# Kernel optimization log

Hardware: AMD Instinct MI355X
Metric: run time of the kernel (lower is better)

Reference implementation:

```python
import jax, jax.numpy as jnp
import numpy as np

NUM_TEAMS = 100000
INPUT_SIZE = 128
HIDDEN = 128
NUM_MATCHES = 1000000
OUT = 3


def setup_inputs() -> dict:
    key = jax.random.key(0)
    ks = jax.random.split(key, 10)
    s_ih = 1.0 / np.sqrt(HIDDEN)
    inputs = jax.random.normal(ks[0], (NUM_TEAMS, INPUT_SIZE), dtype=jnp.float32)
    hx = jax.random.normal(ks[1], (NUM_TEAMS, HIDDEN), dtype=jnp.float32)
    cx = jax.random.normal(ks[2], (NUM_TEAMS, HIDDEN), dtype=jnp.float32)
    matches = jax.random.randint(ks[3], (NUM_MATCHES, 2), 0, NUM_TEAMS, dtype=jnp.int64)
    W_ih = jax.random.uniform(ks[4], (4 * HIDDEN, INPUT_SIZE), jnp.float32, -s_ih, s_ih)
    W_hh = jax.random.uniform(ks[5], (4 * HIDDEN, HIDDEN), jnp.float32, -s_ih, s_ih)
    b_ih = jax.random.uniform(ks[6], (4 * HIDDEN,), jnp.float32, -s_ih, s_ih)
    b_hh = jax.random.uniform(ks[7], (4 * HIDDEN,), jnp.float32, -s_ih, s_ih)
    s_o = 1.0 / np.sqrt(2 * HIDDEN)
    W_out = jax.random.uniform(ks[8], (OUT, 2 * HIDDEN), jnp.float32, -s_o, s_o)
    b_out = jax.random.uniform(ks[9], (OUT,), jnp.float32, -s_o, s_o)
    return {"inputs": inputs, "hx": hx, "cx": cx, "matches": matches,
            "W_ih": W_ih, "W_hh": W_hh, "b_ih": b_ih, "b_hh": b_hh,
            "W_out": W_out, "b_out": b_out}


def reference(inputs, hx, cx, matches, W_ih, W_hh, b_ih, b_hh, W_out, b_out):
    # Batched LSTMCell step across all teams (replaces per-team Python loop).
    gates = inputs @ W_ih.T + b_ih + hx @ W_hh.T + b_hh  # [T, 4H]
    i_g, f_g, g_g, o_g = jnp.split(gates, 4, axis=1)
    c_new = jax.nn.sigmoid(f_g) * cx + jax.nn.sigmoid(i_g) * jnp.tanh(g_g)
    h_new = jax.nn.sigmoid(o_g) * jnp.tanh(c_new)  # [T, H]
    # Fused gather + concat + linear + softmax for all matches.
    home = h_new[matches[:, 0]]  # [M, H]
    away = h_new[matches[:, 1]]  # [M, H]
    feat = jnp.concatenate([home, away], axis=1)  # [M, 2H]
    logits = feat @ W_out.T + b_out  # [M, 3]
    pmf = jax.nn.softmax(logits, axis=-1)
    return pmf
```

## Files before the change

kernel.cpp:

```cpp
#include <hip/hip_runtime.h>
#include <hip/hip_bf16.h>

typedef __bf16 bf16x8 __attribute__((ext_vector_type(8)));
typedef float f32x4 __attribute__((ext_vector_type(4)));

#define NUM_TEAMS 100000
#define NUM_MATCHES 1000000
#define LOG2E 1.4426950408889634f
#define NWG 6250
#define XQ 781
#define XR 2

__device__ __forceinline__ unsigned short f2bf(float x) {
    __hip_bfloat16 h = __float2bfloat16(x);
    return reinterpret_cast<unsigned short&>(h);
}
__device__ __forceinline__ unsigned int cvtpk(float a, float b) {
    unsigned int r;
    asm("v_cvt_pk_bf16_f32 %0, %1, %2" : "=v"(r) : "v"(a), "v"(b));
    return r;
}
__device__ __forceinline__ float exp2_(float x) {
    float r; asm("v_exp_f32 %0, %1" : "=v"(r) : "v"(x)); return r;
}
__device__ __forceinline__ float rcp_(float x) {
    float r; asm("v_rcp_f32 %0, %1" : "=v"(r) : "v"(x)); return r;
}
__device__ __forceinline__ void load_lds16(const float* g, float* l) {
    __builtin_amdgcn_global_load_lds(
        (const __attribute__((address_space(1))) void*)g,
        (__attribute__((address_space(3))) void*)l, 16, 0, 0);
}

__global__ __launch_bounds__(256) void prep_kernel(
    const float* __restrict__ W_ih, const float* __restrict__ W_hh,
    const float* __restrict__ b_ih, const float* __restrict__ b_hh,
    unsigned short* __restrict__ Wpk, float* __restrict__ biasc)
{
    int gid = blockIdx.x * 256 + threadIdx.x;
    int e = gid & 7;
    int chunk = gid >> 3;
    int l15 = chunk & 15;
    int l4 = (chunk >> 4) & 3;
    int rest = chunk >> 6;
    int ks = rest & 7;
    int gate = (rest >> 3) & 3;
    int G = rest >> 5;
    int row = gate * 128 + G * 16 + l15;
    int k = ks * 32 + l4 * 8 + e;
    float v = (k < 128) ? W_ih[row * 128 + k] : W_hh[row * 128 + (k - 128)];
    Wpk[gid] = f2bf(v);
    if (gid < 512) {
        float b = b_ih[gid] + b_hh[gid];
        float scale = ((gid >> 7) == 2) ? (2.0f * LOG2E) : (-LOG2E);
        biasc[gid] = b * scale;
    }
}

__global__ __launch_bounds__(256, 5) void lstm_kernel(
    const float* __restrict__ inputs, const float* __restrict__ hx,
    const float* __restrict__ cx, const unsigned short* __restrict__ Wpk,
    const float* __restrict__ biasc, const float* __restrict__ W_out,
    float* __restrict__ projP)
{
    __shared__ __align__(16) unsigned short Abf[32 * 256];
    __shared__ __align__(16) float cxl[8 * 260];
    __shared__ float Wlds[768];
    const int tid = threadIdx.x;

    const int orig = blockIdx.x;
    const int xcd = orig & 7, idx = orig >> 3;
    const int wgid = (xcd < XR ? xcd * (XQ + 1) : XR * (XQ + 1) + (xcd - XR) * XQ) + idx;
    const int tile = wgid >> 1, ch = wgid & 1;
    const int brow = tile * 32;

    const int lane = tid & 63;
    const int w = tid >> 6;
    const int l15 = lane & 15, l4 = lane >> 4;
    const int hl = w * 16 + l15;
    const int hcol = ch * 64 + hl;

    {
        #pragma unroll
        for (int p = 0; p < 2; ++p) {
            int team = brow + p * 16 + w * 4 + l4;
            load_lds16(cx + (size_t)team * 128 + ch * 64 + l15 * 4,
                       cxl + (p * 4 + w) * 260 + lane * 4);
        }
    }

    {
        const int r0 = tid >> 4, seg = tid & 15;
        const float* srcb = (seg < 8) ? inputs + seg * 16 : hx + (seg - 8) * 16;
        char* lbw = reinterpret_cast<char*>(Abf);
        const int swz = (r0 & 7) << 4;
        #pragma unroll
        for (int p = 0; p < 2; ++p) {
            int r = p * 16 + r0;
            const float* src = srcb + (size_t)(brow + r) * 128;
            float4 v0 = *reinterpret_cast<const float4*>(src);
            float4 v1 = *reinterpret_cast<const float4*>(src + 4);
            float4 v2 = *reinterpret_cast<const float4*>(src + 8);
            float4 v3 = *reinterpret_cast<const float4*>(src + 12);
            int base = r * 512 + seg * 32;
            uint4 q0, q1;
            q0.x = cvtpk(v0.x, v0.y); q0.y = cvtpk(v0.z, v0.w);
            q0.z = cvtpk(v1.x, v1.y); q0.w = cvtpk(v1.z, v1.w);
            q1.x = cvtpk(v2.x, v2.y); q1.y = cvtpk(v2.z, v2.w);
            q1.z = cvtpk(v3.x, v3.y); q1.w = cvtpk(v3.z, v3.w);
            *reinterpret_cast<uint4*>(lbw + (base ^ swz)) = q0;
            *reinterpret_cast<uint4*>(lbw + ((base + 16) ^ swz)) = q1;
        }
        Wlds[tid] = W_out[tid];
        Wlds[256 + tid] = W_out[256 + tid];
        Wlds[512 + tid] = W_out[512 + tid];
    }

    const unsigned short* bpg = Wpk + (size_t)(ch * 4 + w) * 16384 + lane * 8;
    const float bic = biasc[hcol];
    const float bfc = biasc[128 + hcol];
    const float bgc = biasc[256 + hcol];
    const float boc = biasc[384 + hcol];
    const int swzA = (l15 & 7) << 4;
    const int kf = l4 * 16;
    const char* pArow = reinterpret_cast<const char*>(Abf) + l15 * 512;

    f32x4 acc[2][4] = {};

    __syncthreads();

    #pragma unroll
    for (int ks = 0; ks < 8; ++ks) {
        bf16x8 b0 = *(const bf16x8*)(bpg + ks * 512);
        bf16x8 b1 = *(const bf16x8*)(bpg + 4096 + ks * 512);
        bf16x8 b2 = *(const bf16x8*)(bpg + 8192 + ks * 512);
        bf16x8 b3 = *(const bf16x8*)(bpg + 12288 + ks * 512);
        const int ko = (ks * 64 + kf) ^ swzA;
        #pragma unroll
        for (int m = 0; m < 2; ++m) {
            bf16x8 af = *(const bf16x8*)(pArow + m * 8192 + ko);
            acc[m][0] = __builtin_amdgcn_mfma_f32_16x16x32_bf16(af, b0, acc[m][0], 0, 0, 0);
            acc[m][1] = __builtin_amdgcn_mfma_f32_16x16x32_bf16(af, b1, acc[m][1], 0, 0, 0);
            acc[m][2] = __builtin_amdgcn_mfma_f32_16x16x32_bf16(af, b2, acc[m][2], 0, 0, 0);
            acc[m][3] = __builtin_amdgcn_mfma_f32_16x16x32_bf16(af, b3, acc[m][3], 0, 0, 0);
        }
    }

    __syncthreads();

    {
        char* lb = reinterpret_cast<char*>(Abf);
        #pragma unroll
        for (int m = 0; m < 2; ++m) {
            #pragma unroll
            for (int j = 0; j < 4; ++j) {
                float cxv = cxl[(m * 4 + l4) * 260 + j * 64 + hl];
                float si = rcp_(1.0f + exp2_(fmaf(acc[m][0][j], -LOG2E, bic)));
                float sf = rcp_(1.0f + exp2_(fmaf(acc[m][1][j], -LOG2E, bfc)));
                float tg = fmaf(-2.0f, rcp_(1.0f + exp2_(fmaf(acc[m][2][j], 2.0f * LOG2E, bgc))), 1.0f);
                float so = rcp_(1.0f + exp2_(fmaf(acc[m][3][j], -LOG2E, boc)));
                float cn = fmaf(sf, cxv, si * tg);
                float tc = fmaf(-2.0f, rcp_(1.0f + exp2_(cn * (2.0f * LOG2E))), 1.0f);
                float hn = so * tc;
                int t = m * 16 + l4 * 4 + j;
                *reinterpret_cast<float*>(lb + ((t * 256 + hl * 4) ^ ((t & 7) << 4))) = hn;
            }
        }
    }
    __syncthreads();

    {
        int tl = tid >> 3, sub = tid & 7;
        const char* lb = reinterpret_cast<const char*>(Abf);
        int hbase = tl * 256 + sub * 32;
        int hswz = (tl & 7) << 4;
        float a0 = 0.f, a1 = 0.f, a2 = 0.f, a3 = 0.f, a4 = 0.f, a5 = 0.f;
        #pragma unroll
        for (int c = 0; c < 2; ++c) {
            f32x4 h4 = *reinterpret_cast<const f32x4*>(lb + ((hbase + c * 16) ^ hswz));
            #pragma unroll
            for (int i = 0; i < 4; ++i) {
                float h = h4[i];
                int col = ch * 64 + sub * 8 + c * 4 + i;
                a0 += h * Wlds[col];       a1 += h * Wlds[256 + col]; a2 += h * Wlds[512 + col];
                a3 += h * Wlds[128 + col]; a4 += h * Wlds[384 + col]; a5 += h * Wlds[640 + col];
            }
        }
        a0 += __shfl_xor(a0, 1); a1 += __shfl_xor(a1, 1); a2 += __shfl_xor(a2, 1);
        a3 += __shfl_xor(a3, 1); a4 += __shfl_xor(a4, 1); a5 += __shfl_xor(a5, 1);
        a0 += __shfl_xor(a0, 2); a1 += __shfl_xor(a1, 2); a2 += __shfl_xor(a2, 2);
        a3 += __shfl_xor(a3, 2); a4 += __shfl_xor(a4, 2); a5 += __shfl_xor(a5, 2);
        a0 += __shfl_xor(a0, 4); a1 += __shfl_xor(a1, 4); a2 += __shfl_xor(a2, 4);
        a3 += __shfl_xor(a3, 4); a4 += __shfl_xor(a4, 4); a5 += __shfl_xor(a5, 4);
        int team = brow + tl;
        if (sub == 0) {
            float4* o = reinterpret_cast<float4*>(projP + (size_t)team * 16 + ch * 8);
            o[0] = make_float4(a0, a1, a2, a2);
            o[1] = make_float4(a3, a4, a5, a5);
        }
    }
}

__global__ __launch_bounds__(256) void match_kernel(
    const int* __restrict__ matches, const float* __restrict__ projP,
    const float* __restrict__ b_out, float* __restrict__ out)
{
    int m = blockIdx.x * 256 + threadIdx.x;
    if (m >= NUM_MATCHES) return;
    int2 mi = reinterpret_cast<const int2*>(matches)[m];
    const float4* pp = reinterpret_cast<const float4*>(projP);
    float4 h0 = pp[(size_t)mi.x * 4 + 0];
    float4 h1 = pp[(size_t)mi.x * 4 + 2];
    float4 a0 = pp[(size_t)mi.y * 4 + 1];
    float4 a1 = pp[(size_t)mi.y * 4 + 3];
    float l0 = h0.x + h1.x + a0.x + a1.x + b_out[0];
    float l1 = h0.y + h1.y + a0.y + a1.y + b_out[1];
    float l2 = h0.z + h1.z + a0.z + a1.z + b_out[2];
    float mx = fmaxf(l0, fmaxf(l1, l2));
    float e0 = __expf(l0 - mx), e1 = __expf(l1 - mx), e2 = __expf(l2 - mx);
    float inv = 1.0f / (e0 + e1 + e2);
    out[3 * m + 0] = e0 * inv;
    out[3 * m + 1] = e1 * inv;
    out[3 * m + 2] = e2 * inv;
}

extern "C" void kernel_launch(void* const* d_in, const int* in_sizes, int n_in,
                              void* d_out, int out_size, void* d_ws, size_t ws_size,
                              hipStream_t stream) {
    const float* inputs = (const float*)d_in[0];
    const float* hx     = (const float*)d_in[1];
    const float* cx     = (const float*)d_in[2];
    const int*   matches= (const int*)d_in[3];
    const float* W_ih   = (const float*)d_in[4];
    const float* W_hh   = (const float*)d_in[5];
    const float* b_ih   = (const float*)d_in[6];
    const float* b_hh   = (const float*)d_in[7];
    const float* W_out  = (const float*)d_in[8];
    const float* b_out  = (const float*)d_in[9];
    float* out = (float*)d_out;

    char* ws = (char*)d_ws;
    unsigned short* Wpk  = (unsigned short*)ws;
    float* biasc         = (float*)(ws + 262144);
    float* projP         = (float*)(ws + (1 << 20));

    prep_kernel <<<512, 256, 0, stream>>>(W_ih, W_hh, b_ih, b_hh, Wpk, biasc);
    lstm_kernel <<<NWG, 256, 0, stream>>>(inputs, hx, cx, Wpk, biasc, W_out, projP);
    match_kernel<<<(NUM_MATCHES + 255) / 256, 256, 0, stream>>>(matches, projP, b_out, out);
}
```

Baseline: 82.12 us.

## Compute both hidden halves per workgroup and halve projection gather traffic

Each workgroup now handles all 128 hidden columns of its 32-team tile in two passes instead of splitting the columns across two workgroups. The two half-projections are summed in registers, so projP shrinks to 8 floats per team and the match kernel gathers two float4 per match instead of four. cx is now read straight into registers instead of through an async LDS load, and each tile's inputs and hx rows are converted to bf16 only once. In exchange the grid is halved, which lowers parallelism, and each workgroup runs longer with more serialised MFMA and activation work.

Measured after the change: 156.0 us. 1.9x slower.

```diff
diff --git a/kernel.cpp b/kernel.cpp
--- a/kernel.cpp
+++ b/kernel.cpp
@@ -7,9 +7,9 @@
 #define NUM_TEAMS 100000
 #define NUM_MATCHES 1000000
 #define LOG2E 1.4426950408889634f
-#define NWG 6250
-#define XQ 781
-#define XR 2
+#define NWG 3125
+#define XQ 390
+#define XR 5
 
 __device__ __forceinline__ unsigned short f2bf(float x) {
     __hip_bfloat16 h = __float2bfloat16(x);
@@ -25,11 +25,6 @@
 }
 __device__ __forceinline__ float rcp_(float x) {
     float r; asm("v_rcp_f32 %0, %1" : "=v"(r) : "v"(x)); return r;
-}
-__device__ __forceinline__ void load_lds16(const float* g, float* l) {
-    __builtin_amdgcn_global_load_lds(
-        (const __attribute__((address_space(1))) void*)g,
-        (__attribute__((address_space(3))) void*)l, 16, 0, 0);
 }
 
 __global__ __launch_bounds__(256) void prep_kernel(
@@ -64,140 +59,156 @@
     float* __restrict__ projP)
 {
     __shared__ __align__(16) unsigned short Abf[32 * 256];
-    __shared__ __align__(16) float cxl[8 * 260];
+    __shared__ __align__(16) float Hf[32 * 64];
     __shared__ float Wlds[768];
     const int tid = threadIdx.x;
 
     const int orig = blockIdx.x;
     const int xcd = orig & 7, idx = orig >> 3;
-    const int wgid = (xcd < XR ? xcd * (XQ + 1) : XR * (XQ + 1) + (xcd - XR) * XQ) + idx;
-    const int tile = wgid >> 1, ch = wgid & 1;
+    const int tile = (xcd < XR ? xcd * (XQ + 1) : XR * (XQ + 1) + (xcd - XR) * XQ) + idx;
     const int brow = tile * 32;
 
     const int lane = tid & 63;
     const int w = tid >> 6;
     const int l15 = lane & 15, l4 = lane >> 4;
     const int hl = w * 16 + l15;
-    const int hcol = ch * 64 + hl;
 
     {
-        #pragma unroll
-        for (int p = 0; p < 2; ++p) {
-            int team = brow + p * 16 + w * 4 + l4;
-            load_lds16(cx + (size_t)team * 128 + ch * 64 + l15 * 4,
-                       cxl + (p * 4 + w) * 260 + lane * 4);
-        }
-    }
-
-    {
-        const int r0 = tid >> 4, seg = tid & 15;
-        const float* srcb = (seg < 8) ? inputs + seg * 16 : hx + (seg - 8) * 16;
+        const int r = tid >> 3, seg = tid & 7;
+        const float* src = ((seg < 4) ? inputs + seg * 32 : hx + (seg - 4) * 32)
+                           + (size_t)(brow + r) * 128;
+        float4 v0 = *reinterpret_cast<const float4*>(src);
+        float4 v1 = *reinterpret_cast<const float4*>(src + 4);
+        float4 v2 = *reinterpret_cast<const float4*>(src + 8);
+        float4 v3 = *reinterpret_cast<const float4*>(src + 12);
+        float4 v4 = *reinterpret_cast<const float4*>(src + 16);
+        float4 v5 = *reinterpret_cast<const float4*>(src + 20);
+        float4 v6 = *reinterpret_cast<const float4*>(src + 24);
+        float4 v7 = *reinterpret_cast<const float4*>(src + 28);
         char* lbw = reinterpret_cast<char*>(Abf);
-        const int swz = (r0 & 7) << 4;
-        #pragma unroll
-        for (int p = 0; p < 2; ++p) {
-            int r = p * 16 + r0;
-            const float* src = srcb + (size_t)(brow + r) * 128;
-            float4 v0 = *reinterpret_cast<const float4*>(src);
-            float4 v1 = *reinterpret_cast<const float4*>(src + 4);
-            float4 v2 = *reinterpret_cast<const float4*>(src + 8);
-            float4 v3 = *reinterpret_cast<const float4*>(src + 12);
-            int base = r * 512 + seg * 32;
-            uint4 q0, q1;
-            q0.x = cvtpk(v0.x, v0.y); q0.y = cvtpk(v0.z, v0.w);
-            q0.z = cvtpk(v1.x, v1.y); q0.w = cvtpk(v1.z, v1.w);
-            q1.x = cvtpk(v2.x, v2.y); q1.y = cvtpk(v2.z, v2.w);
-            q1.z = cvtpk(v3.x, v3.y); q1.w = cvtpk(v3.z, v3.w);
-            *reinterpret_cast<uint4*>(lbw + (base ^ swz)) = q0;
-            *reinterpret_cast<uint4*>(lbw + ((base + 16) ^ swz)) = q1;
-        }
+        const int base = r * 512 + seg * 64;
+        const int swz = (r & 7) << 4;
+        uint4 q0, q1;
+        q0.x = cvtpk(v0.x, v0.y); q0.y = cvtpk(v0.z, v0.w);
+        q0.z = cvtpk(v1.x, v1.y); q0.w = cvtpk(v1.z, v1.w);
+        q1.x = cvtpk(v2.x, v2.y); q1.y = cvtpk(v2.z, v2.w);
+        q1.z = cvtpk(v3.x, v3.y); q1.w = cvtpk(v3.z, v3.w);
+        *reinterpret_cast<uint4*>(lbw + (base ^ swz)) = q0;
+        *reinterpret_cast<uint4*>(lbw + ((base + 16) ^ swz)) = q1;
+        q0.x = cvtpk(v4.x, v4.y); q0.y = cvtpk(v4.z, v4.w);
+        q0.z = cvtpk(v5.x, v5.y); q0.w = cvtpk(v5.z, v5.w);
+        q1.x = cvtpk(v6.x, v6.y); q1.y = cvtpk(v6.z, v6.w);
+        q1.z = cvtpk(v7.x, v7.y); q1.w = cvtpk(v7.z, v7.w);
+        *reinterpret_cast<uint4*>(lbw + ((base + 32) ^ swz)) = q0;
+        *reinterpret_cast<uint4*>(lbw + ((base + 48) ^ swz)) = q1;
         Wlds[tid] = W_out[tid];
         Wlds[256 + tid] = W_out[256 + tid];
         Wlds[512 + tid] = W_out[512 + tid];
     }
 
-    const unsigned short* bpg = Wpk + (size_t)(ch * 4 + w) * 16384 + lane * 8;
-    const float bic = biasc[hcol];
-    const float bfc = biasc[128 + hcol];
-    const float bgc = biasc[256 + hcol];
-    const float boc = biasc[384 + hcol];
+    float cxa[8];
+    #pragma unroll
+    for (int m = 0; m < 2; ++m)
+        #pragma unroll
+        for (int j = 0; j < 4; ++j)
+            cxa[m * 4 + j] = cx[(size_t)(brow + m * 16 + l4 * 4 + j) * 128 + hl];
+
     const int swzA = (l15 & 7) << 4;
     const int kf = l4 * 16;
     const char* pArow = reinterpret_cast<const char*>(Abf) + l15 * 512;
 
-    f32x4 acc[2][4] = {};
+    float p0, p1, p2, p3, p4, p5;
 
     __syncthreads();
 
     #pragma unroll
-    for (int ks = 0; ks < 8; ++ks) {
-        bf16x8 b0 = *(const bf16x8*)(bpg + ks * 512);
-        bf16x8 b1 = *(const bf16x8*)(bpg + 4096 + ks * 512);
-        bf16x8 b2 = *(const bf16x8*)(bpg + 8192 + ks * 512);
-        bf16x8 b3 = *(const bf16x8*)(bpg + 12288 + ks * 512);
-        const int ko = (ks * 64 + kf) ^ swzA;
+    for (int ch = 0; ch < 2; ++ch) {
+        const int hcol = ch * 64 + hl;
+        const unsigned short* bpg = Wpk + (size_t)(ch * 4 + w) * 16384 + lane * 8;
+        const float bic = biasc[hcol];
+        const float bfc = biasc[128 + hcol];
+        const float bgc = biasc[256 + hcol];
+        const float boc = biasc[384 + hcol];
+
+        f32x4 acc[2][4] = {};
         #pragma unroll
-        for (int m = 0; m < 2; ++m) {
-            bf16x8 af = *(const bf16x8*)(pArow + m * 8192 + ko);
-            acc[m][0] = __builtin_amdgcn_mfma_f32_16x16x32_bf16(af, b0, acc[m][0], 0, 0, 0);
-            acc[m][1] = __builtin_amdgcn_mfma_f32_16x16x32_bf16(af, b1, acc[m][1], 0, 0, 0);
-            acc[m][2] = __builtin_amdgcn_mfma_f32_16x16x32_bf16(af, b2, acc[m][2], 0, 0, 0);
-            acc[m][3] = __builtin_amdgcn_mfma_f32_16x16x32_bf16(af, b3, acc[m][3], 0, 0, 0);
-        }
-    }
-
-    __syncthreads();
-
-    {
-        char* lb = reinterpret_cast<char*>(Abf);
-        #pragma unroll
-        for (int m = 0; m < 2; ++m) {
-            #pragma unroll
-            for (int j = 0; j < 4; ++j) {
-                float cxv = cxl[(m * 4 + l4) * 260 + j * 64 + hl];
-                float si = rcp_(1.0f + exp2_(fmaf(acc[m][0][j], -LOG2E, bic)));
-                float sf = rcp_(1.0f + exp2_(fmaf(acc[m][1][j], -LOG2E, bfc)));
-                float tg = fmaf(-2.0f, rcp_(1.0f + exp2_(fmaf(acc[m][2][j], 2.0f * LOG2E, bgc))), 1.0f);
-                float so = rcp_(1.0f + exp2_(fmaf(acc[m][3][j], -LOG2E, boc)));
-                float cn = fmaf(sf, cxv, si * tg);
-                float tc = fmaf(-2.0f, rcp_(1.0f + exp2_(cn * (2.0f * LOG2E))), 1.0f);
-                float hn = so * tc;
-                int t = m * 16 + l4 * 4 + j;
-                *reinterpret_cast<float*>(lb + ((t * 256 + hl * 4) ^ ((t & 7) << 4))) = hn;
-            }
-        }
-    }
-    __syncthreads();
-
-    {
-        int tl = tid >> 3, sub = tid & 7;
-        const char* lb = reinterpret_cast<const char*>(Abf);
-        int hbase = tl * 256 + sub * 32;
-        int hswz = (tl & 7) << 4;
-        float a0 = 0.f, a1 = 0.f, a2 = 0.f, a3 = 0.f, a4 = 0.f, a5 = 0.f;
-        #pragma unroll
-        for (int c = 0; c < 2; ++c) {
-            f32x4 h4 = *reinterpret_cast<const f32x4*>(lb + ((hbase + c * 16) ^ hswz));
-            #pragma unroll
-            for (int i = 0; i < 4; ++i) {
-                float h = h4[i];
-                int col = ch * 64 + sub * 8 + c * 4 + i;
-                a0 += h * Wlds[col];       a1 += h * Wlds[256 + col]; a2 += h * Wlds[512 + col];
-                a3 += h * Wlds[128 + col]; a4 += h * Wlds[384 + col]; a5 += h * Wlds[640 + col];
-            }
-        }
-        a0 += __shfl_xor(a0, 1); a1 += __shfl_xor(a1, 1); a2 += __shfl_xor(a2, 1);
-        a3 += __shfl_xor(a3, 1); a4 += __shfl_xor(a4, 1); a5 += __shfl_xor(a5, 1);
-        a0 += __shfl_xor(a0, 2); a1 += __shfl_xor(a1, 2); a2 += __shfl_xor(a2, 2);
-        a3 += __shfl_xor(a3, 2); a4 += __shfl_xor(a4, 2); a5 += __shfl_xor(a5, 2);
-        a0 += __shfl_xor(a0, 4); a1 += __shfl_xor(a1, 4); a2 += __shfl_xor(a2, 4);
-        a3 += __shfl_xor(a3, 4); a4 += __shfl_xor(a4, 4); a5 += __shfl_xor(a5, 4);
-        int team = brow + tl;
-        if (sub == 0) {
-            float4* o = reinterpret_cast<float4*>(projP + (size_t)team * 16 + ch * 8);
-            o[0] = make_float4(a0, a1, a2, a2);
-            o[1] = make_float4(a3, a4, a5, a5);
-        }
+        for (int ks = 0; ks < 8; ++ks) {
+            bf16x8 b0 = *(const bf16x8*)(bpg + ks * 512);
+            bf16x8 b1 = *(const bf16x8*)(bpg + 4096 + ks * 512);
+            bf16x8 b2 = *(const bf16x8*)(bpg + 8192 + ks * 512);
+            bf16x8 b3 = *(const bf16x8*)(bpg + 12288 + ks * 512);
+            const int ko = (ks * 64 + kf) ^ swzA;
+            #pragma unroll
+            for (int m = 0; m < 2; ++m) {
+                bf16x8 af = *(const bf16x8*)(pArow + m * 8192 + ko);
+                acc[m][0] = __builtin_amdgcn_mfma_f32_16x16x32_bf16(af, b0, acc[m][0], 0, 0, 0);
+                acc[m][1] = __builtin_amdgcn_mfma_f32_16x16x32_bf16(af, b1, acc[m][1], 0, 0, 0);
+                acc[m][2] = __builtin_amdgcn_mfma_f32_16x16x32_bf16(af, b2, acc[m][2], 0, 0, 0);
+                acc[m][3] = __builtin_amdgcn_mfma_f32_16x16x32_bf16(af, b3, acc[m][3], 0, 0, 0);
+            }
+        }
+
+        {
+            char* lb = reinterpret_cast<char*>(Hf);
+            #pragma unroll
+            for (int m = 0; m < 2; ++m) {
+                #pragma unroll
+                for (int j = 0; j < 4; ++j) {
+                    float si = rcp_(1.0f + exp2_(fmaf(acc[m][0][j], -LOG2E, bic)));
+                    float sf = rcp_(1.0f + exp2_(fmaf(acc[m][1][j], -LOG2E, bfc)));
+                    float tg = fmaf(-2.0f, rcp_(1.0f + exp2_(fmaf(acc[m][2][j], 2.0f * LOG2E, bgc))), 1.0f);
+                    float so = rcp_(1.0f + exp2_(fmaf(acc[m][3][j], -LOG2E, boc)));
+                    float cn = fmaf(sf, cxa[m * 4 + j], si * tg);
+                    float tc = fmaf(-2.0f, rcp_(1.0f + exp2_(cn * (2.0f * LOG2E))), 1.0f);
+                    float hn = so * tc;
+                    int t = m * 16 + l4 * 4 + j;
+                    *reinterpret_cast<float*>(lb + ((t * 256 + hl * 4) ^ ((t & 7) << 4))) = hn;
+                }
+            }
+        }
+
+        if (ch == 0) {
+            #pragma unroll
+            for (int m = 0; m < 2; ++m)
+                #pragma unroll
+                for (int j = 0; j < 4; ++j)
+                    cxa[m * 4 + j] = cx[(size_t)(brow + m * 16 + l4 * 4 + j) * 128 + 64 + hl];
+        }
+
+        __syncthreads();
+
+        {
+            int tl = tid >> 3, sub = tid & 7;
+            const char* lb = reinterpret_cast<const char*>(Hf);
+            int hbase = tl * 256 + sub * 32;
+            int hswz = (tl & 7) << 4;
+            float a0 = 0.f, a1 = 0.f, a2 = 0.f, a3 = 0.f, a4 = 0.f, a5 = 0.f;
+            #pragma unroll
+            for (int c = 0; c < 2; ++c) {
+                f32x4 h4 = *reinterpret_cast<const f32x4*>(lb + ((hbase + c * 16) ^ hswz));
+                #pragma unroll
+                for (int i = 0; i < 4; ++i) {
+                    float h = h4[i];
+                    int col = ch * 64 + sub * 8 + c * 4 + i;
+                    a0 += h * Wlds[col];       a1 += h * Wlds[256 + col]; a2 += h * Wlds[512 + col];
+                    a3 += h * Wlds[128 + col]; a4 += h * Wlds[384 + col]; a5 += h * Wlds[640 + col];
+                }
+            }
+            a0 += __shfl_xor(a0, 1); a1 += __shfl_xor(a1, 1); a2 += __shfl_xor(a2, 1);
+            a3 += __shfl_xor(a3, 1); a4 += __shfl_xor(a4, 1); a5 += __shfl_xor(a5, 1);
+            a0 += __shfl_xor(a0, 2); a1 += __shfl_xor(a1, 2); a2 += __shfl_xor(a2, 2);
+            a3 += __shfl_xor(a3, 2); a4 += __shfl_xor(a4, 2); a5 += __shfl_xor(a5, 2);
+            a0 += __shfl_xor(a0, 4); a1 += __shfl_xor(a1, 4); a2 += __shfl_xor(a2, 4);
+            a3 += __shfl_xor(a3, 4); a4 += __shfl_xor(a4, 4); a5 += __shfl_xor(a5, 4);
+            if (ch == 0) {
+                p0 = a0; p1 = a1; p2 = a2; p3 = a3; p4 = a4; p5 = a5;
+            } else if (sub == 0) {
+                float4* o = reinterpret_cast<float4*>(projP + (size_t)(brow + tl) * 8);
+                o[0] = make_float4(p0 + a0, p1 + a1, p2 + a2, p2 + a2);
+                o[1] = make_float4(p3 + a3, p4 + a4, p5 + a5, p5 + a5);
+            }
+        }
+        if (ch == 0) __syncthreads();
     }
 }
 
@@ -209,13 +220,11 @@
     if (m >= NUM_MATCHES) return;
     int2 mi = reinterpret_cast<const int2*>(matches)[m];
     const float4* pp = reinterpret_cast<const float4*>(projP);
-    float4 h0 = pp[(size_t)mi.x * 4 + 0];
-    float4 h1 = pp[(size_t)mi.x * 4 + 2];
-    float4 a0 = pp[(size_t)mi.y * 4 + 1];
-    float4 a1 = pp[(size_t)mi.y * 4 + 3];
-    float l0 = h0.x + h1.x + a0.x + a1.x + b_out[0];
-    float l1 = h0.y + h1.y + a0.y + a1.y + b_out[1];
-    float l2 = h0.z + h1.z + a0.z + a1.z + b_out[2];
+    float4 hv = pp[(size_t)mi.x * 2 + 0];
+    float4 av = pp[(size_t)mi.y * 2 + 1];
+    float l0 = hv.x + av.x + b_out[0];
+    float l1 = hv.y + av.y + b_out[1];
+    float l2 = hv.z + av.z + b_out[2];
     float mx = fmaxf(l0, fmaxf(l1, l2));
     float e0 = __expf(l0 - mx), e1 = __expf(l1 - mx), e2 = __expf(l2 - mx);
     float inv = 1.0f / (e0 + e1 + e2);
```
